# Kernel tuning notes

Hardware: AMD Instinct MI355X
Metric: run time of the kernel (lower is better)

The kernel has to match this reference:

```python
import jax, jax.numpy as jnp
import numpy as np

B = 1024
P = 9            # patch_length
D = 2700         # d_model = input_dims = 30*30*3, num_heads=1 so d_k = D
DFF = 512
EPS = 1e-5


def setup_inputs() -> dict:
    key = jax.random.key(0)
    ks = jax.random.split(key, 32)
    s = 0.02
    inp = {
        "state": jax.random.normal(ks[0], (B, P * D), jnp.float32),
        "H1": jax.random.normal(ks[1], (B, P, DFF), jnp.float32),
        "H2": jax.random.normal(ks[2], (B, P, DFF), jnp.float32),
        # main projections: (in, out) layout for x @ W
        "Wq": jax.random.normal(ks[3], (D, D), jnp.float32) * s,
        "bq": jnp.zeros((D,), jnp.float32),
        "Wk": jax.random.normal(ks[4], (D, D), jnp.float32) * s,
        "bk": jnp.zeros((D,), jnp.float32),
        "Wv": jax.random.normal(ks[5], (D, D), jnp.float32) * s,
        "bv": jnp.zeros((D,), jnp.float32),
        # aux modulation projections from dff -> d_model
        "WC1q": jax.random.normal(ks[6], (DFF, D), jnp.float32) * s,
        "bC1q": jnp.zeros((D,), jnp.float32),
        "WC1k": jax.random.normal(ks[7], (DFF, D), jnp.float32) * s,
        "bC1k": jnp.zeros((D,), jnp.float32),
        "WC1v": jax.random.normal(ks[8], (DFF, D), jnp.float32) * s,
        "bC1v": jnp.zeros((D,), jnp.float32),
        "WC2q": jax.random.normal(ks[9], (DFF, D), jnp.float32) * s,
        "bC2q": jnp.zeros((D,), jnp.float32),
        "WC2k": jax.random.normal(ks[10], (DFF, D), jnp.float32) * s,
        "bC2k": jnp.zeros((D,), jnp.float32),
        "WC2v": jax.random.normal(ks[11], (DFF, D), jnp.float32) * s,
        "bC2v": jnp.zeros((D,), jnp.float32),
        # LayerNorm (norm1) affine params
        "gamma": jnp.ones((D,), jnp.float32),
        "beta": jnp.zeros((D,), jnp.float32),
    }
    return inp


def _layernorm(x, gamma, beta):
    mu = jnp.mean(x, axis=-1, keepdims=True)
    var = jnp.mean(jnp.square(x - mu), axis=-1, keepdims=True)
    return (x - mu) * jax.lax.rsqrt(var + EPS) * gamma + beta


def reference(state, H1, H2, Wq, bq, Wk, bk, Wv, bv,
              WC1q, bC1q, WC1k, bC1k, WC1v, bC1v,
              WC2q, bC2q, WC2k, bC2k, WC2v, bC2v,
              gamma, beta):
    x = state.reshape(-1, P, D)  # (B, 9, 2700)
    # elementwise-modulated Q/K/V (num_heads == 1)
    q = (x @ Wq + bq) * ((H1 @ WC1q + bC1q) + (H2 @ WC2q + bC2q))
    k = (x @ Wk + bk) * ((H1 @ WC1k + bC1k) + (H2 @ WC2k + bC2k))
    v = (x @ Wv + bv) * ((H1 @ WC1v + bC1v) + (H2 @ WC2v + bC2v))
    scale = 1.0 / jnp.sqrt(jnp.asarray(D, jnp.float32))
    scores = jnp.einsum("bqd,bkd->bqk", q, k) * scale  # (B, 9, 9)
    A = jax.nn.softmax(scores, axis=-1)
    attn = jnp.einsum("bqk,bkd->bqd", A, v)
    Z1 = x + attn  # dropout is identity in eval
    return _layernorm(Z1, gamma, beta)
```

## Files before the change

### kernel.cpp

```cpp
#include <hip/hip_runtime.h>
#include <stdint.h>


#define MROWS  9216
#define NCOLS  8192
#define KP1    2752
#define KP2    1024
#define DMODEL 2700

typedef __bf16 bf16x8 __attribute__((ext_vector_type(8)));
typedef float  f32x4  __attribute__((ext_vector_type(4)));

__device__ __forceinline__ float b2f(unsigned short u) {
  union { unsigned int u; float f; } v; v.u = ((unsigned int)u) << 16; return v.f;
}
__device__ __forceinline__ unsigned short f2b(float f) {
  union { float f; unsigned int u; } v; v.f = f;
  unsigned int r = v.u + 0x7FFFu + ((v.u >> 16) & 1u);
  return (unsigned short)(r >> 16);
}

__device__ __forceinline__ void gl2lds16(const void* g, void* l) {
  __builtin_amdgcn_global_load_lds(
      (const __attribute__((address_space(1))) void*)g,
      (__attribute__((address_space(3))) void*)l, 16, 0, 0);
}


__global__ void cvt_x(const float* __restrict__ src, unsigned short* __restrict__ dst) {
  int idx = blockIdx.x * 256 + threadIdx.x;
  int r = idx / KP1;
  int c = idx - r * KP1;
  float v = (c < DMODEL) ? src[(size_t)r * DMODEL + c] : 0.f;
  dst[idx] = f2b(v);
}

__global__ void cvt_h(const float* __restrict__ H1, const float* __restrict__ H2,
                      unsigned short* __restrict__ dst) {
  int idx = blockIdx.x * 256 + threadIdx.x;
  int r = idx >> 10, c = idx & 1023;
  float v = (c < 512) ? H1[r * 512 + c] : H2[r * 512 + (c - 512)];
  dst[idx] = f2b(v);
}

__global__ void cvt_wqkv(const float* __restrict__ Wq, const float* __restrict__ Wk,
                         const float* __restrict__ Wv, unsigned short* __restrict__ Wt) {
  __shared__ float tile[32][33];
  int k0 = blockIdx.x * 32, n0 = blockIdx.y * 32;
  int tx = threadIdx.x, ty = threadIdx.y;
#pragma unroll
  for (int s = 0; s < 4; s++) {
    int kk = k0 + ty + 8 * s, nn = n0 + tx;
    float v = 0.f;
    if (kk < DMODEL && nn < 3 * DMODEL) {
      int sec = (nn >= 5400) ? 2 : ((nn >= 2700) ? 1 : 0);
      int d = nn - sec * DMODEL;
      const float* W = (sec == 0) ? Wq : ((sec == 1) ? Wk : Wv);
      v = W[(size_t)kk * DMODEL + d];
    }
    tile[ty + 8 * s][tx] = v;
  }
  __syncthreads();
#pragma unroll
  for (int s = 0; s < 4; s++) {
    int nn = n0 + ty + 8 * s, kk = k0 + tx;
    Wt[(size_t)nn * KP1 + kk] = f2b(tile[tx][ty + 8 * s]);
  }
}

__global__ void cvt_wc(const float* __restrict__ C1q, const float* __restrict__ C1k,
                       const float* __restrict__ C1v, const float* __restrict__ C2q,
                       const float* __restrict__ C2k, const float* __restrict__ C2v,
                       unsigned short* __restrict__ Wt) {
  __shared__ float tile[32][33];
  int k0 = blockIdx.x * 32, n0 = blockIdx.y * 32;
  int tx = threadIdx.x, ty = threadIdx.y;
#pragma unroll
  for (int s = 0; s < 4; s++) {
    int kk = k0 + ty + 8 * s, nn = n0 + tx;
    float v = 0.f;
    if (nn < 3 * DMODEL) {
      int sec = (nn >= 5400) ? 2 : ((nn >= 2700) ? 1 : 0);
      int d = nn - sec * DMODEL;
      const float* W;
      int kr = kk;
      if (kk < 512) {
        W = (sec == 0) ? C1q : ((sec == 1) ? C1k : C1v);
      } else {
        W = (sec == 0) ? C2q : ((sec == 1) ? C2k : C2v);
        kr = kk - 512;
      }
      v = W[(size_t)kr * DMODEL + d];
    }
    tile[ty + 8 * s][tx] = v;
  }
  __syncthreads();
#pragma unroll
  for (int s = 0; s < 4; s++) {
    int nn = n0 + ty + 8 * s, kk = k0 + tx;
    Wt[(size_t)nn * KP2 + kk] = f2b(tile[tx][ty + 8 * s]);
  }
}

__global__ __launch_bounds__(256, 2) void gemm_fused(
    const unsigned short* __restrict__ Xb,
    const unsigned short* __restrict__ Wt,
    const unsigned short* __restrict__ Hb,
    const unsigned short* __restrict__ WCt,
    unsigned short* __restrict__ MQ,
    const float* __restrict__ bq_, const float* __restrict__ bk_, const float* __restrict__ bv_,
    const float* __restrict__ b1q, const float* __restrict__ b1k, const float* __restrict__ b1v,
    const float* __restrict__ b2q, const float* __restrict__ b2k, const float* __restrict__ b2v)
{
  __shared__ __align__(16) unsigned short As[128 * 64];
  __shared__ __align__(16) unsigned short Bs[128 * 64];
  const int tid = threadIdx.x;
  const int wave = tid >> 6, lane = tid & 63;
  const int m0 = blockIdx.y * 128, n0 = blockIdx.x * 128;
  const int wm = (wave >> 1) * 64, wn = (wave & 1) * 64;
  const int lm = lane & 15, lq = lane >> 4, l7 = lane & 7;

  int prow[4], pcl[4];
  unsigned int ldsoff[4];
#pragma unroll
  for (int r = 0; r < 4; r++) {
    int p = r * 256 + tid;
    prow[r] = p >> 3;
    pcl[r] = ((p & 7) ^ (prow[r] & 7)) * 8;
    ldsoff[r] = (unsigned int)p * 8;
  }

  f32x4 acc[4][4];
#pragma unroll
  for (int i = 0; i < 4; i++)
#pragma unroll
    for (int j = 0; j < 4; j++) acc[i][j] = (f32x4){0.f, 0.f, 0.f, 0.f};

  for (int k0 = 0; k0 < KP2; k0 += 64) {
#pragma unroll
    for (int r = 0; r < 4; r++) {
      gl2lds16(Hb + (size_t)(m0 + prow[r]) * KP2 + pcl[r] + k0, As + ldsoff[r]);
      gl2lds16(WCt + (size_t)(n0 + prow[r]) * KP2 + pcl[r] + k0, Bs + ldsoff[r]);
    }
    __syncthreads();
#pragma unroll
    for (int c = 0; c < 2; c++) {
      bf16x8 af[4], bfr[4];
      const int kx = (c * 4 + lq) ^ l7;
#pragma unroll
      for (int t = 0; t < 4; t++) {
        af[t]  = *(const bf16x8*)(As + (((wm + t * 16 + lm) << 3) + kx) * 8);
        bfr[t] = *(const bf16x8*)(Bs + (((wn + t * 16 + lm) << 3) + kx) * 8);
      }
#pragma unroll
      for (int mt = 0; mt < 4; mt++)
#pragma unroll
        for (int nt = 0; nt < 4; nt++)
          acc[mt][nt] = __builtin_amdgcn_mfma_f32_16x16x32_bf16(
              af[mt], bfr[nt], acc[mt][nt], 0, 0, 0);
    }
    __syncthreads();
  }

  unsigned int modp[4][4][2];
#pragma unroll
  for (int nt = 0; nt < 4; nt++) {
    int gc = n0 + wn + nt * 16 + lm;
    float bmod = 0.f;
    if (gc < 3 * DMODEL) {
      int sec = (gc >= 5400) ? 2 : ((gc >= 2700) ? 1 : 0);
      int d = gc - sec * DMODEL;
      const float* u1 = (sec == 0) ? b1q : ((sec == 1) ? b1k : b1v);
      const float* u2 = (sec == 0) ? b2q : ((sec == 1) ? b2k : b2v);
      bmod = u1[d] + u2[d];
    }
#pragma unroll
    for (int mt = 0; mt < 4; mt++) {
#pragma unroll
      for (int h = 0; h < 2; h++) {
        unsigned int lo = f2b(acc[mt][nt][2 * h] + bmod);
        unsigned int hi = f2b(acc[mt][nt][2 * h + 1] + bmod);
        modp[mt][nt][h] = lo | (hi << 16);
      }
    }
  }
#pragma unroll
  for (int i = 0; i < 4; i++)
#pragma unroll
    for (int j = 0; j < 4; j++) acc[i][j] = (f32x4){0.f, 0.f, 0.f, 0.f};

  for (int k0 = 0; k0 < KP1; k0 += 64) {
#pragma unroll
    for (int r = 0; r < 4; r++) {
      gl2lds16(Xb + (size_t)(m0 + prow[r]) * KP1 + pcl[r] + k0, As + ldsoff[r]);
      gl2lds16(Wt + (size_t)(n0 + prow[r]) * KP1 + pcl[r] + k0, Bs + ldsoff[r]);
    }
    __syncthreads();
#pragma unroll
    for (int c = 0; c < 2; c++) {
      bf16x8 af[4], bfr[4];
      const int kx = (c * 4 + lq) ^ l7;
#pragma unroll
      for (int t = 0; t < 4; t++) {
        af[t]  = *(const bf16x8*)(As + (((wm + t * 16 + lm) << 3) + kx) * 8);
        bfr[t] = *(const bf16x8*)(Bs + (((wn + t * 16 + lm) << 3) + kx) * 8);
      }
#pragma unroll
      for (int mt = 0; mt < 4; mt++)
#pragma unroll
        for (int nt = 0; nt < 4; nt++)
          acc[mt][nt] = __builtin_amdgcn_mfma_f32_16x16x32_bf16(
              af[mt], bfr[nt], acc[mt][nt], 0, 0, 0);
    }
    __syncthreads();
  }

#pragma unroll
  for (int nt = 0; nt < 4; nt++) {
    int gc = n0 + wn + nt * 16 + lm;
    float bmv = 0.f;
    if (gc < 3 * DMODEL) {
      int sec = (gc >= 5400) ? 2 : ((gc >= 2700) ? 1 : 0);
      int d = gc - sec * DMODEL;
      const float* bm = (sec == 0) ? bq_ : ((sec == 1) ? bk_ : bv_);
      bmv = bm[d];
    }
#pragma unroll
    for (int mt = 0; mt < 4; mt++) {
      int grb = m0 + wm + mt * 16 + lq * 4;
#pragma unroll
      for (int i = 0; i < 4; i++) {
        float mod = b2f((unsigned short)(modp[mt][nt][i >> 1] >> ((i & 1) * 16)));
        MQ[(size_t)(grb + i) * NCOLS + gc] = f2b((acc[mt][nt][i] + bmv) * mod);
      }
    }
  }
}

__global__ __launch_bounds__(256, 2) void attn_ln(
    const unsigned short* __restrict__ qkv,
    const float* __restrict__ x,
    const float* __restrict__ gamma, const float* __restrict__ beta,
    float* __restrict__ out)
{
  __shared__ float part[4][81];
  __shared__ float sc[81];
  __shared__ float redS[4][9], redQ[4][9];
  __shared__ float muL[9], rsL[9];

  const int b = blockIdx.x;
  const int tid = threadIdx.x, wave = tid >> 6, lane = tid & 63;
  const unsigned short* qb = qkv + (size_t)b * 9 * NCOLS;

  {
    const int l15 = lane & 15, lq8 = (lane >> 4) * 8;
    const int rA = (l15 < 9) ? l15 : 8;
    const unsigned short* qrow = qb + (size_t)rA * NCOLS;
    const unsigned short* krow = qb + (size_t)rA * NCOLS + DMODEL;
    f32x4 accS = (f32x4){0.f, 0.f, 0.f, 0.f};
    for (int s = wave; s < 85; s += 4) {
      int k0 = s * 32 + lq8;
      union { uint2 u[2]; unsigned int w[4]; bf16x8 v; } au, bu;
      au.u[0] = *(const uint2*)(qrow + k0);
      au.u[1] = *(const uint2*)(qrow + k0 + 4);
      bu.u[0] = *(const uint2*)(krow + k0);
      bu.u[1] = *(const uint2*)(krow + k0 + 4);
      if (s == 84) {
#pragma unroll
        for (int wd = 0; wd < 4; wd++)
          if (k0 + 2 * wd >= DMODEL) { au.w[wd] = 0u; bu.w[wd] = 0u; }
      }
      accS = __builtin_amdgcn_mfma_f32_16x16x32_bf16(au.v, bu.v, accS, 0, 0, 0);
    }
#pragma unroll
    for (int i = 0; i < 4; i++) {
      int row = (lane >> 4) * 4 + i, col = l15;
      if (row < 9 && col < 9) part[wave][row * 9 + col] = accS[i];
    }
  }
  __syncthreads();

  if (tid < 81)
    sc[tid] = (part[0][tid] + part[1][tid] + part[2][tid] + part[3][tid])
              * 0.019245008972987526f;
  __syncthreads();

  if (tid < 9) {
    float mx = -1e30f;
#pragma unroll
    for (int j = 0; j < 9; j++) mx = fmaxf(mx, sc[tid * 9 + j]);
    float e[9], sum = 0.f;
#pragma unroll
    for (int j = 0; j < 9; j++) { e[j] = __expf(sc[tid * 9 + j] - mx); sum += e[j]; }
    float inv = 1.f / sum;
#pragma unroll
    for (int j = 0; j < 9; j++) sc[tid * 9 + j] = e[j] * inv;
  }
  __syncthreads();

  float sum[9], sq[9];
#pragma unroll
  for (int i = 0; i < 9; i++) { sum[i] = 0.f; sq[i] = 0.f; }
  unsigned int pv[9][3][2];
#pragma unroll
  for (int c = 0; c < 3; c++) {
    int e = tid + c * 256;
    if (e < 675) {
      float4 t4[9];
#pragma unroll
      for (int i = 0; i < 9; i++)
        t4[i] = ((const float4*)(x + (size_t)(b * 9 + i) * DMODEL))[e];
#pragma unroll
      for (int j = 0; j < 9; j++) {
        ushort4 vv = ((const ushort4*)(qb + (size_t)j * NCOLS + 5400))[e];
        float v0 = b2f(vv.x), v1 = b2f(vv.y), v2 = b2f(vv.z), v3 = b2f(vv.w);
#pragma unroll
        for (int i = 0; i < 9; i++) {
          float p = sc[i * 9 + j];
          t4[i].x += p * v0; t4[i].y += p * v1;
          t4[i].z += p * v2; t4[i].w += p * v3;
        }
      }
#pragma unroll
      for (int i = 0; i < 9; i++) {
        sum[i] += t4[i].x + t4[i].y + t4[i].z + t4[i].w;
        sq[i]  += t4[i].x * t4[i].x + t4[i].y * t4[i].y
                + t4[i].z * t4[i].z + t4[i].w * t4[i].w;
        pv[i][c][0] = (unsigned int)f2b(t4[i].x) | ((unsigned int)f2b(t4[i].y) << 16);
        pv[i][c][1] = (unsigned int)f2b(t4[i].z) | ((unsigned int)f2b(t4[i].w) << 16);
      }
    }
  }

#pragma unroll
  for (int i = 0; i < 9; i++) {
    float s = sum[i], q = sq[i];
#pragma unroll
    for (int off = 32; off > 0; off >>= 1) {
      s += __shfl_down(s, off, 64);
      q += __shfl_down(q, off, 64);
    }
    if (lane == 0) { redS[wave][i] = s; redQ[wave][i] = q; }
  }
  __syncthreads();
  if (tid < 9) {
    float ts = redS[0][tid] + redS[1][tid] + redS[2][tid] + redS[3][tid];
    float tq = redQ[0][tid] + redQ[1][tid] + redQ[2][tid] + redQ[3][tid];
    float mu = ts * (1.f / 2700.f);
    muL[tid] = mu;
    rsL[tid] = rsqrtf(tq * (1.f / 2700.f) - mu * mu + 1e-5f);
  }
  __syncthreads();

#pragma unroll
  for (int c = 0; c < 3; c++) {
    int e = tid + c * 256;
    if (e < 675) {
      float4 g = ((const float4*)gamma)[e];
      float4 bb = ((const float4*)beta)[e];
#pragma unroll
      for (int i = 0; i < 9; i++) {
        float m = muL[i], r = rsL[i];
        float t0 = b2f((unsigned short)(pv[i][c][0] & 0xFFFF));
        float t1 = b2f((unsigned short)(pv[i][c][0] >> 16));
        float t2 = b2f((unsigned short)(pv[i][c][1] & 0xFFFF));
        float t3 = b2f((unsigned short)(pv[i][c][1] >> 16));
        float4 o;
        o.x = (t0 - m) * r * g.x + bb.x;
        o.y = (t1 - m) * r * g.y + bb.y;
        o.z = (t2 - m) * r * g.z + bb.z;
        o.w = (t3 - m) * r * g.w + bb.w;
        ((float4*)(out + (size_t)(b * 9 + i) * DMODEL))[e] = o;
      }
    }
  }
}

extern "C" void kernel_launch(void* const* d_in, const int* in_sizes, int n_in,
                              void* d_out, int out_size, void* d_ws, size_t ws_size,
                              hipStream_t stream) {
  const float* state = (const float*)d_in[0];
  const float* H1    = (const float*)d_in[1];
  const float* H2    = (const float*)d_in[2];
  const float* Wq    = (const float*)d_in[3];
  const float* bq    = (const float*)d_in[4];
  const float* Wk    = (const float*)d_in[5];
  const float* bk    = (const float*)d_in[6];
  const float* Wv    = (const float*)d_in[7];
  const float* bv    = (const float*)d_in[8];
  const float* WC1q  = (const float*)d_in[9];
  const float* bC1q  = (const float*)d_in[10];
  const float* WC1k  = (const float*)d_in[11];
  const float* bC1k  = (const float*)d_in[12];
  const float* WC1v  = (const float*)d_in[13];
  const float* bC1v  = (const float*)d_in[14];
  const float* WC2q  = (const float*)d_in[15];
  const float* bC2q  = (const float*)d_in[16];
  const float* WC2k  = (const float*)d_in[17];
  const float* bC2k  = (const float*)d_in[18];
  const float* WC2v  = (const float*)d_in[19];
  const float* bC2v  = (const float*)d_in[20];
  const float* gamma = (const float*)d_in[21];
  const float* beta  = (const float*)d_in[22];
  float* out = (float*)d_out;

  char* ws = (char*)d_ws;
  unsigned short* Xb  = (unsigned short*)(ws + 0);
  unsigned short* Wt  = (unsigned short*)(ws + 50724864);
  unsigned short* Hb  = (unsigned short*)(ws + 95813632);
  unsigned short* WCt = (unsigned short*)(ws + 114688000);
  unsigned short* MQ  = (unsigned short*)(ws + 131465216);

  cvt_x<<<dim3(MROWS * KP1 / 256), dim3(256), 0, stream>>>(state, Xb);
  cvt_wqkv<<<dim3(KP1 / 32, NCOLS / 32), dim3(32, 8), 0, stream>>>(Wq, Wk, Wv, Wt);
  cvt_h<<<dim3(MROWS * KP2 / 256), dim3(256), 0, stream>>>(H1, H2, Hb);
  cvt_wc<<<dim3(KP2 / 32, NCOLS / 32), dim3(32, 8), 0, stream>>>(WC1q, WC1k, WC1v,
                                                                 WC2q, WC2k, WC2v, WCt);

  gemm_fused<<<dim3(NCOLS / 128, MROWS / 128), dim3(256), 0, stream>>>(
      Xb, Wt, Hb, WCt, MQ, bq, bk, bv, bC1q, bC1k, bC1v, bC2q, bC2k, bC2v);

  attn_ln<<<dim3(1024), dim3(256), 0, stream>>>(MQ, state, gamma, beta, out);
}
```

Measured before the change: 1.109 ms.

## Split fused GEMM into two 256x256-tile pipelined kernels with MQ round-trip

Replaces the single 128x128-tile fused GEMM with two kernels that use 256x256 tiles, 8 waves, double-buffered LDS with a ping-pong quarter-tile schedule, setprio around the MFMA blocks, and a swizzled block order for L2 locality. The modulation GEMM now writes bf16 results to MQ, and the main GEMM reads them back to multiply, so the modulation values no longer live in registers. The larger tiles and overlapped loads are meant to raise MFMA utilisation and cut global traffic per FLOP. The cost is an extra global write and read of the modulation tensor plus one more launch.

```diff
diff --git a/kernel.cpp b/kernel.cpp
--- a/kernel.cpp
+++ b/kernel.cpp
@@ -102,136 +102,240 @@
   }
 }
 
-__global__ __launch_bounds__(256, 2) void gemm_fused(
-    const unsigned short* __restrict__ Xb,
-    const unsigned short* __restrict__ Wt,
-    const unsigned short* __restrict__ Hb,
-    const unsigned short* __restrict__ WCt,
+
+#define BAR() __builtin_amdgcn_s_barrier()
+
+template<int NT, int KS>
+__device__ __forceinline__ void gemm8_core(
+    unsigned short (&lds)[2][2][16384],
+    const unsigned short* __restrict__ Ab,
+    const unsigned short* __restrict__ Bb,
+    f32x4 (&acc)[8][4],
+    int tid, int wm, int wn, int lm, int lq, int l7)
+{
+  bf16x8 af[2][4], bfr[2][2];
+
+  auto stage = [&](int buf, int op, int h, int t) {
+    const unsigned short* s = (op ? Bb : Ab) + (size_t)(h * 128) * KS + (size_t)(t * 64);
+    unsigned short* d = &lds[buf][op][h * 128 * 64 + tid * 8];
+    gl2lds16(s, d);
+    gl2lds16(s + (size_t)64 * KS, d + 4096);
+  };
+  auto fragsA = [&](int buf, int MH) {
+#pragma unroll
+    for (int c = 0; c < 2; c++) {
+      const int kx = ((c * 4 + lq) ^ l7) * 8;
+#pragma unroll
+      for (int t = 0; t < 4; t++)
+        af[c][t] = *(const bf16x8*)&lds[buf][0][(wm + MH * 64 + t * 16 + lm) * 64 + kx];
+    }
+  };
+  auto fragsB = [&](int buf, int NH) {
+#pragma unroll
+    for (int c = 0; c < 2; c++) {
+      const int kx = ((c * 4 + lq) ^ l7) * 8;
+#pragma unroll
+      for (int t = 0; t < 2; t++)
+        bfr[c][t] = *(const bf16x8*)&lds[buf][1][(wn + (NH * 2 + t) * 16 + lm) * 64 + kx];
+    }
+  };
+  auto mfmas = [&](int MH, int NH) {
+    asm volatile("s_waitcnt lgkmcnt(0)" ::: "memory");
+    __builtin_amdgcn_sched_barrier(0);
+    __builtin_amdgcn_s_setprio(1);
+#pragma unroll
+    for (int c = 0; c < 2; c++)
+#pragma unroll
+      for (int mt = 0; mt < 4; mt++)
+#pragma unroll
+        for (int nt = 0; nt < 2; nt++)
+          acc[MH * 4 + mt][NH * 2 + nt] = __builtin_amdgcn_mfma_f32_16x16x32_bf16(
+              af[c][mt], bfr[c][nt], acc[MH * 4 + mt][NH * 2 + nt], 0, 0, 0);
+    __builtin_amdgcn_s_setprio(0);
+  };
+
+  stage(0, 0, 0, 0); stage(0, 0, 1, 0); stage(0, 1, 0, 0); stage(0, 1, 1, 0);
+
+  const int nfull = NT >> 1;
+#pragma unroll 1
+  for (int j = 0; j < nfull; ++j) {
+    const int t1 = 2 * j + 1, t2 = 2 * j + 2;
+
+    stage(1, 0, 0, t1);
+    asm volatile("s_waitcnt vmcnt(2)" ::: "memory");
+    BAR();
+    fragsA(0, 0); fragsB(0, 0); mfmas(0, 0);
+    BAR();
+
+    fragsB(0, 1); stage(1, 0, 1, t1);
+    BAR();
+    mfmas(0, 1);
+    BAR();
+
+    fragsA(0, 1); stage(1, 1, 0, t1);
+    BAR();
+    mfmas(1, 1);
+    BAR();
+
+    fragsB(0, 0); stage(1, 1, 1, t1);
+    BAR();
+    mfmas(1, 0);
+    BAR();
+
+    if (t2 < NT) {
+      stage(0, 0, 0, t2);
+      asm volatile("s_waitcnt vmcnt(2)" ::: "memory");
+      BAR();
+      fragsA(1, 0); fragsB(1, 0); mfmas(0, 0);
+      BAR();
+
+      fragsB(1, 1); stage(0, 0, 1, t2);
+      BAR();
+      mfmas(0, 1);
+      BAR();
+
+      fragsA(1, 1); stage(0, 1, 0, t2);
+      BAR();
+      mfmas(1, 1);
+      BAR();
+
+      fragsB(1, 0); stage(0, 1, 1, t2);
+      BAR();
+      mfmas(1, 0);
+      BAR();
+    } else {
+      asm volatile("s_waitcnt vmcnt(0)" ::: "memory");
+      BAR();
+      fragsA(1, 0); fragsB(1, 0); mfmas(0, 0);
+      BAR();
+      fragsB(1, 1); mfmas(0, 1);
+      BAR();
+      fragsA(1, 1); mfmas(1, 1);
+      BAR();
+      fragsB(1, 0); mfmas(1, 0);
+      BAR();
+    }
+  }
+  if (NT & 1) {
+    asm volatile("s_waitcnt vmcnt(0)" ::: "memory");
+    BAR();
+    fragsA(0, 0); fragsB(0, 0); mfmas(0, 0);
+    BAR();
+    fragsB(0, 1); mfmas(0, 1);
+    BAR();
+    fragsA(0, 1); mfmas(1, 1);
+    BAR();
+    fragsB(0, 0); mfmas(1, 0);
+    BAR();
+  }
+}
+
+__global__ __launch_bounds__(512, 2) void gemm8_mod(
+    const unsigned short* __restrict__ Hb, const unsigned short* __restrict__ WCt,
     unsigned short* __restrict__ MQ,
-    const float* __restrict__ bq_, const float* __restrict__ bk_, const float* __restrict__ bv_,
     const float* __restrict__ b1q, const float* __restrict__ b1k, const float* __restrict__ b1v,
     const float* __restrict__ b2q, const float* __restrict__ b2k, const float* __restrict__ b2v)
 {
-  __shared__ __align__(16) unsigned short As[128 * 64];
-  __shared__ __align__(16) unsigned short Bs[128 * 64];
+  __shared__ __attribute__((aligned(16))) unsigned short lds[2][2][16384];
   const int tid = threadIdx.x;
   const int wave = tid >> 6, lane = tid & 63;
-  const int m0 = blockIdx.y * 128, n0 = blockIdx.x * 128;
-  const int wm = (wave >> 1) * 64, wn = (wave & 1) * 64;
+  const int wm = (wave >> 2) * 128, wn = (wave & 3) * 64;
   const int lm = lane & 15, lq = lane >> 4, l7 = lane & 7;
-
-  int prow[4], pcl[4];
-  unsigned int ldsoff[4];
-#pragma unroll
-  for (int r = 0; r < 4; r++) {
-    int p = r * 256 + tid;
-    prow[r] = p >> 3;
-    pcl[r] = ((p & 7) ^ (prow[r] & 7)) * 8;
-    ldsoff[r] = (unsigned int)p * 8;
-  }
-
-  f32x4 acc[4][4];
-#pragma unroll
-  for (int i = 0; i < 4; i++)
+  const int wg = blockIdx.x;
+  const int swz = (wg & 7) * 144 + (wg >> 3);
+  const int m0 = (swz >> 5) * 256, n0 = (swz & 31) * 256;
+  const int sr = tid >> 3;
+  const int skb = ((tid & 7) ^ (sr & 7)) * 8;
+
+  const unsigned short* Ab = Hb  + (size_t)(m0 + sr) * KP2 + skb;
+  const unsigned short* Bb = WCt + (size_t)(n0 + sr) * KP2 + skb;
+
+  f32x4 acc[8][4];
+#pragma unroll
+  for (int i = 0; i < 8; i++)
 #pragma unroll
     for (int j = 0; j < 4; j++) acc[i][j] = (f32x4){0.f, 0.f, 0.f, 0.f};
 
-  for (int k0 = 0; k0 < KP2; k0 += 64) {
-#pragma unroll
-    for (int r = 0; r < 4; r++) {
-      gl2lds16(Hb + (size_t)(m0 + prow[r]) * KP2 + pcl[r] + k0, As + ldsoff[r]);
-      gl2lds16(WCt + (size_t)(n0 + prow[r]) * KP2 + pcl[r] + k0, Bs + ldsoff[r]);
-    }
-    __syncthreads();
-#pragma unroll
-    for (int c = 0; c < 2; c++) {
-      bf16x8 af[4], bfr[4];
-      const int kx = (c * 4 + lq) ^ l7;
-#pragma unroll
-      for (int t = 0; t < 4; t++) {
-        af[t]  = *(const bf16x8*)(As + (((wm + t * 16 + lm) << 3) + kx) * 8);
-        bfr[t] = *(const bf16x8*)(Bs + (((wn + t * 16 + lm) << 3) + kx) * 8);
-      }
-#pragma unroll
-      for (int mt = 0; mt < 4; mt++)
-#pragma unroll
-        for (int nt = 0; nt < 4; nt++)
-          acc[mt][nt] = __builtin_amdgcn_mfma_f32_16x16x32_bf16(
-              af[mt], bfr[nt], acc[mt][nt], 0, 0, 0);
-    }
-    __syncthreads();
-  }
-
-  unsigned int modp[4][4][2];
+  gemm8_core<16, KP2>(lds, Ab, Bb, acc, tid, wm, wn, lm, lq, l7);
+
+  float bmod[4];
 #pragma unroll
   for (int nt = 0; nt < 4; nt++) {
     int gc = n0 + wn + nt * 16 + lm;
-    float bmod = 0.f;
+    float v = 0.f;
     if (gc < 3 * DMODEL) {
       int sec = (gc >= 5400) ? 2 : ((gc >= 2700) ? 1 : 0);
       int d = gc - sec * DMODEL;
       const float* u1 = (sec == 0) ? b1q : ((sec == 1) ? b1k : b1v);
       const float* u2 = (sec == 0) ? b2q : ((sec == 1) ? b2k : b2v);
-      bmod = u1[d] + u2[d];
-    }
-#pragma unroll
-    for (int mt = 0; mt < 4; mt++) {
-#pragma unroll
-      for (int h = 0; h < 2; h++) {
-        unsigned int lo = f2b(acc[mt][nt][2 * h] + bmod);
-        unsigned int hi = f2b(acc[mt][nt][2 * h + 1] + bmod);
-        modp[mt][nt][h] = lo | (hi << 16);
-      }
-    }
-  }
-#pragma unroll
-  for (int i = 0; i < 4; i++)
+      v = u1[d] + u2[d];
+    }
+    bmod[nt] = v;
+  }
+#pragma unroll
+  for (int mt = 0; mt < 8; mt++) {
+    int grb = m0 + wm + mt * 16 + lq * 4;
+#pragma unroll
+    for (int nt = 0; nt < 4; nt++) {
+      int gc = n0 + wn + nt * 16 + lm;
+#pragma unroll
+      for (int i = 0; i < 4; i++)
+        MQ[(size_t)(grb + i) * NCOLS + gc] = f2b(acc[mt][nt][i] + bmod[nt]);
+    }
+  }
+}
+
+__global__ __launch_bounds__(512, 2) void gemm8_main(
+    const unsigned short* __restrict__ Xb, const unsigned short* __restrict__ Wt,
+    unsigned short* MQ,
+    const float* __restrict__ bq_, const float* __restrict__ bk_, const float* __restrict__ bv_)
+{
+  __shared__ __attribute__((aligned(16))) unsigned short lds[2][2][16384];
+  const int tid = threadIdx.x;
+  const int wave = tid >> 6, lane = tid & 63;
+  const int wm = (wave >> 2) * 128, wn = (wave & 3) * 64;
+  const int lm = lane & 15, lq = lane >> 4, l7 = lane & 7;
+  const int wg = blockIdx.x;
+  const int swz = (wg & 7) * 144 + (wg >> 3);
+  const int m0 = (swz >> 5) * 256, n0 = (swz & 31) * 256;
+  const int sr = tid >> 3;
+  const int skb = ((tid & 7) ^ (sr & 7)) * 8;
+
+  const unsigned short* Ab = Xb + (size_t)(m0 + sr) * KP1 + skb;
+  const unsigned short* Bb = Wt + (size_t)(n0 + sr) * KP1 + skb;
+
+  f32x4 acc[8][4];
+#pragma unroll
+  for (int i = 0; i < 8; i++)
 #pragma unroll
     for (int j = 0; j < 4; j++) acc[i][j] = (f32x4){0.f, 0.f, 0.f, 0.f};
 
-  for (int k0 = 0; k0 < KP1; k0 += 64) {
-#pragma unroll
-    for (int r = 0; r < 4; r++) {
-      gl2lds16(Xb + (size_t)(m0 + prow[r]) * KP1 + pcl[r] + k0, As + ldsoff[r]);
-      gl2lds16(Wt + (size_t)(n0 + prow[r]) * KP1 + pcl[r] + k0, Bs + ldsoff[r]);
-    }
-    __syncthreads();
-#pragma unroll
-    for (int c = 0; c < 2; c++) {
-      bf16x8 af[4], bfr[4];
-      const int kx = (c * 4 + lq) ^ l7;
-#pragma unroll
-      for (int t = 0; t < 4; t++) {
-        af[t]  = *(const bf16x8*)(As + (((wm + t * 16 + lm) << 3) + kx) * 8);
-        bfr[t] = *(const bf16x8*)(Bs + (((wn + t * 16 + lm) << 3) + kx) * 8);
-      }
-#pragma unroll
-      for (int mt = 0; mt < 4; mt++)
-#pragma unroll
-        for (int nt = 0; nt < 4; nt++)
-          acc[mt][nt] = __builtin_amdgcn_mfma_f32_16x16x32_bf16(
-              af[mt], bfr[nt], acc[mt][nt], 0, 0, 0);
-    }
-    __syncthreads();
-  }
-
+  gemm8_core<43, KP1>(lds, Ab, Bb, acc, tid, wm, wn, lm, lq, l7);
+
+  float bmain[4];
 #pragma unroll
   for (int nt = 0; nt < 4; nt++) {
     int gc = n0 + wn + nt * 16 + lm;
-    float bmv = 0.f;
+    float v = 0.f;
     if (gc < 3 * DMODEL) {
       int sec = (gc >= 5400) ? 2 : ((gc >= 2700) ? 1 : 0);
       int d = gc - sec * DMODEL;
       const float* bm = (sec == 0) ? bq_ : ((sec == 1) ? bk_ : bv_);
-      bmv = bm[d];
-    }
-#pragma unroll
-    for (int mt = 0; mt < 4; mt++) {
-      int grb = m0 + wm + mt * 16 + lq * 4;
+      v = bm[d];
+    }
+    bmain[nt] = v;
+  }
+#pragma unroll
+  for (int mt = 0; mt < 8; mt++) {
+    int grb = m0 + wm + mt * 16 + lq * 4;
+#pragma unroll
+    for (int nt = 0; nt < 4; nt++) {
+      int gc = n0 + wn + nt * 16 + lm;
 #pragma unroll
       for (int i = 0; i < 4; i++) {
-        float mod = b2f((unsigned short)(modp[mt][nt][i >> 1] >> ((i & 1) * 16)));
-        MQ[(size_t)(grb + i) * NCOLS + gc] = f2b((acc[mt][nt][i] + bmv) * mod);
+        size_t off = (size_t)(grb + i) * NCOLS + gc;
+        float mod = b2f(MQ[off]);
+        MQ[off] = f2b((acc[mt][nt][i] + bmain[nt]) * mod);
       }
     }
   }
@@ -411,14 +515,17 @@
   unsigned short* WCt = (unsigned short*)(ws + 114688000);
   unsigned short* MQ  = (unsigned short*)(ws + 131465216);
 
-  cvt_x<<<dim3(MROWS * KP1 / 256), dim3(256), 0, stream>>>(state, Xb);
-  cvt_wqkv<<<dim3(KP1 / 32, NCOLS / 32), dim3(32, 8), 0, stream>>>(Wq, Wk, Wv, Wt);
   cvt_h<<<dim3(MROWS * KP2 / 256), dim3(256), 0, stream>>>(H1, H2, Hb);
   cvt_wc<<<dim3(KP2 / 32, NCOLS / 32), dim3(32, 8), 0, stream>>>(WC1q, WC1k, WC1v,
                                                                  WC2q, WC2k, WC2v, WCt);
-
-  gemm_fused<<<dim3(NCOLS / 128, MROWS / 128), dim3(256), 0, stream>>>(
-      Xb, Wt, Hb, WCt, MQ, bq, bk, bv, bC1q, bC1k, bC1v, bC2q, bC2k, bC2v);
+  cvt_x<<<dim3(MROWS * KP1 / 256), dim3(256), 0, stream>>>(state, Xb);
+  cvt_wqkv<<<dim3(KP1 / 32, NCOLS / 32), dim3(32, 8), 0, stream>>>(Wq, Wk, Wv, Wt);
+
+  gemm8_mod<<<dim3(MROWS / 256 * NCOLS / 256), dim3(512), 0, stream>>>(
+      Hb, WCt, MQ, bC1q, bC1k, bC1v, bC2q, bC2k, bC2v);
+
+  gemm8_main<<<dim3(MROWS / 256 * NCOLS / 256), dim3(512), 0, stream>>>(
+      Xb, Wt, MQ, bq, bk, bv);
 
   attn_ln<<<dim3(1024), dim3(256), 0, stream>>>(MQ, state, gamma, beta, out);
 }
```

Measured after the change: 1.696 ms. +52.9%, slower.
